# Performance work log

Measured on AMD Instinct MI355X. Metric: run time of the kernel, lower is better.

The kernel has to match this reference:

```python
import jax, jax.numpy as jnp
from jax import lax
import numpy as np

C_LL = 16      # c = 4**(px_num-1), px_num=2
C_FT = 64      # 4**px_num channels in wavelet feature ft0/ft1
TILE = C_FT // 4


def _conv3(x, w, b):
    # 3x3, stride 1, pad 1 conv in NCHW/OIHW layout
    y = lax.conv_general_dilated(x, w, (1, 1), ((1, 1), (1, 1)),
                                 dimension_numbers=('NCHW', 'OIHW', 'NCHW'))
    return y + b[None, :, None, None]


def setup_inputs() -> dict:
    key = jax.random.key(0)
    ks = jax.random.split(key, 16)
    B, H, W = 4, 256, 256

    def g(k, shape, scale=1.0):
        return jax.random.normal(k, shape, dtype=jnp.float32) * scale

    return {
        'ft0': g(ks[0], (B, C_FT, H, W)),
        'ft1': g(ks[1], (B, C_FT, H, W)),
        'gamma_up': g(ks[2], (B, 4, H, W)),
        'denoise_down': g(ks[3], (B, C_LL, H, W)),
        'coeff_a': jax.random.uniform(ks[4], (1, 1, 1, 1), dtype=jnp.float32),
        'coeff_b': jax.random.uniform(ks[5], (1, 1, 1, 1), dtype=jnp.float32),
        # FusionM: cin=24 -> 64 -> 64 -> 4
        'fw1': g(ks[6], (64, 24, 3, 3), 0.05), 'fb1': jnp.zeros((64,), jnp.float32),
        'fw2': g(ks[7], (64, 64, 3, 3), 0.05), 'fb2': jnp.zeros((64,), jnp.float32),
        'fw3': g(ks[8], (4, 64, 3, 3), 0.05), 'fb3': jnp.zeros((4,), jnp.float32),
        # DenoiseM: cin=100 -> 64 -> 64 -> 64
        'dw1': g(ks[9], (64, 100, 3, 3), 0.05), 'db1': jnp.zeros((64,), jnp.float32),
        'dw2': g(ks[10], (64, 64, 3, 3), 0.05), 'db2': jnp.zeros((64,), jnp.float32),
        'dw3': g(ks[11], (64, 64, 3, 3), 0.05), 'db3': jnp.zeros((64,), jnp.float32),
    }


def reference(ft0, ft1, gamma_up, denoise_down, coeff_a, coeff_b,
              fw1, fb1, fw2, fb2, fw3, fb3,
              dw1, db1, dw2, db2, dw3, db3):
    c = C_LL
    ll0 = ft0[:, :c]
    ll1 = ft1[:, :c]
    sigma_ll0 = jnp.clip(ll0[:, :c // 4], 0.0, 1.0) * coeff_a + coeff_b
    sigma_ll1 = jnp.clip(ll1[:, :c // 4], 0.0, 1.0) * coeff_a + coeff_b

    fusion_in = jnp.concatenate([jnp.abs(ll1 - ll0), gamma_up, sigma_ll1], axis=1)
    h = jax.nn.relu(_conv3(fusion_in, fw1, fb1))
    h = jax.nn.relu(_conv3(h, fw2, fb2))
    gamma = jax.nn.sigmoid(_conv3(h, fw3, fb3))          # [B,4,H,W]

    gammaM = jnp.repeat(gamma, TILE, axis=1)             # [B,64,H,W]
    fusion_out = ft0 * (1.0 - gammaM) + ft1 * gammaM
    sigma = (1.0 - gamma) ** 2 * sigma_ll0 + gamma ** 2 * sigma_ll1

    # DenoiseM
    denoise_in = jnp.concatenate([fusion_out, ll1, denoise_down, sigma], axis=1)  # [B,100,H,W]
    d = jax.nn.relu(_conv3(denoise_in, dw1, db1))
    d = jax.nn.relu(_conv3(d, dw2, db2))
    denoise_out = _conv3(d, dw3, db3)

    return fusion_out, denoise_out, gamma, sigma
```

## Files before the change

### kernel.cpp

```cpp
#include <hip/hip_runtime.h>
#include <stdint.h>

#define HW 65536

typedef __attribute__((ext_vector_type(8))) short short8;
typedef __attribute__((ext_vector_type(4))) float f32x4;
typedef unsigned short u16;

struct __align__(8) us4 { u16 x, y, z, w; };
struct __align__(16) us8 { us4 lo, hi; };

__device__ __forceinline__ u16 f2bf(float f) {
  union { float f; uint32_t u; } v; v.f = f;
  uint32_t r = v.u + 0x7FFFu + ((v.u >> 16) & 1u);
  return (u16)(r >> 16);
}

__device__ __forceinline__ us4 pack4(float a, float b, float c, float d) {
  us4 o; o.x = f2bf(a); o.y = f2bf(b); o.z = f2bf(c); o.w = f2bf(d); return o;
}

__device__ __forceinline__ void reorder_one(int idx, const float* __restrict__ src,
                                            u16* __restrict__ dst, int CO, int CI,
                                            int COp, int Cp) {
  int cc = idx & 7;
  int t = idx >> 3;
  int co = t % COp;
  int u = t / COp;
  int cgn = Cp >> 3;
  int cg = u % cgn;
  int tap = u / cgn;
  int ci = cg * 8 + cc;
  float v = 0.f;
  if (co < CO && ci < CI) v = src[(co * CI + ci) * 9 + tap];
  dst[idx] = f2bf(v);
}

__global__ void prep_k(const float* __restrict__ s1, const float* __restrict__ s2,
                       const float* __restrict__ s3, const float* __restrict__ s4,
                       const float* __restrict__ s5, const float* __restrict__ s6,
                       u16* __restrict__ d1, u16* __restrict__ d2, u16* __restrict__ d3,
                       u16* __restrict__ d4, u16* __restrict__ d5, u16* __restrict__ d6,
                       u16* __restrict__ zrow) {
  int idx = blockIdx.x * 256 + threadIdx.x;
  if (idx < 18432) { reorder_one(idx, s1, d1, 64, 24, 64, 32); return; }
  idx -= 18432;
  if (idx < 36864) { reorder_one(idx, s2, d2, 64, 64, 64, 64); return; }
  idx -= 36864;
  if (idx < 9216)  { reorder_one(idx, s3, d3, 4, 64, 16, 64); return; }
  idx -= 9216;
  if (idx < 73728) { reorder_one(idx, s4, d4, 64, 100, 64, 128); return; }
  idx -= 73728;
  if (idx < 36864) { reorder_one(idx, s5, d5, 64, 64, 64, 64); return; }
  idx -= 36864;
  if (idx < 36864) { reorder_one(idx, s6, d6, 64, 64, 64, 64); return; }
  idx -= 36864;
  zrow[idx] = 0;
}

__global__ void fusion_in_k(const float* __restrict__ ft0, const float* __restrict__ ft1,
                            const float* __restrict__ gup, const float* __restrict__ ca,
                            const float* __restrict__ cb, u16* __restrict__ fin) {
  const int p = blockIdx.x * 256 + threadIdx.x;
  const int n = p >> 16;
  const int pp = p & 65535;
  const float* b0 = ft0 + (size_t)n * 64 * HW + pp;
  const float* b1 = ft1 + (size_t)n * 64 * HW + pp;
  const float a = ca[0], bb = cb[0];
  u16* base = fin + ((size_t)(n * 256 + (pp >> 8)) * 4 * 256 + (pp & 255)) * 8;
  us8 o;
#pragma unroll
  for (int cg = 0; cg < 2; ++cg) {
    float v[8];
#pragma unroll
    for (int r = 0; r < 8; ++r) {
      const int ch = cg * 8 + r;
      v[r] = fabsf(b1[ch * HW] - b0[ch * HW]);
    }
    o.lo = pack4(v[0], v[1], v[2], v[3]);
    o.hi = pack4(v[4], v[5], v[6], v[7]);
    *(us8*)(base + cg * 2048) = o;
  }
  const float* gu = gup + (size_t)n * 4 * HW + pp;
  o.lo = pack4(gu[0], gu[HW], gu[2 * HW], gu[3 * HW]);
  o.hi = pack4(fminf(fmaxf(b1[0 * HW], 0.f), 1.f) * a + bb,
               fminf(fmaxf(b1[1 * HW], 0.f), 1.f) * a + bb,
               fminf(fmaxf(b1[2 * HW], 0.f), 1.f) * a + bb,
               fminf(fmaxf(b1[3 * HW], 0.f), 1.f) * a + bb);
  *(us8*)(base + 2 * 2048) = o;
  const us4 zz = {0, 0, 0, 0};
  o.lo = zz; o.hi = zz;
  *(us8*)(base + 3 * 2048) = o;
}

template <int CIN, int MT, int OMODE>
__global__ __launch_bounds__(512, 1) void conv3_k(
    const u16* __restrict__ in, const u16* __restrict__ wr,
    const float* __restrict__ bias, const u16* __restrict__ zrow,
    u16* __restrict__ obf, float* __restrict__ of32,
    const float* __restrict__ ft0, const float* __restrict__ ft1,
    const float* __restrict__ dd, const float* __restrict__ ca,
    const float* __restrict__ cb, float* __restrict__ fo_out,
    float* __restrict__ si_out, u16* __restrict__ din) {
  constexpr int M = MT * 16;
  constexpr int NCH = CIN / 32;
  constexpr int NREG = 16;
  constexpr int RSTR = 259;
  __shared__ __align__(16) u16 Blds[2 * NREG * RSTR * 8];
  const int tid = threadIdx.x;
  const int w = tid >> 6;
  const int lane = tid & 63;
  const int l15 = lane & 15;
  const int quad = lane >> 4;
  const int yo = w >> 2;
  const int wq = w & 3;

  const int b = blockIdx.x;
  const int i = b >> 3;
  const int n = i >> 4;
  const int ytile = ((b & 7) << 4) + (i & 15);
  const int y0 = ytile * 2;

  f32x4 acc[MT][4];
#pragma unroll
  for (int mt = 0; mt < MT; ++mt)
#pragma unroll
    for (int nt = 0; nt < 4; ++nt) acc[mt][nt] = (f32x4){0.f, 0.f, 0.f, 0.f};

  const u16* inb = in + (size_t)n * HW * CIN;
  const u16* rp[4];
#pragma unroll
  for (int r = 0; r < 4; ++r) {
    const int y2 = y0 + r - 1;
    rp[r] = (y2 >= 0 && y2 < 256) ? (inb + (size_t)y2 * 256 * CIN) : zrow;
  }
  if (tid < 64) {
    const int bf = tid >> 5;
    const int reg = (tid >> 1) & 15;
    const int sl = (tid & 1) * 257;
    *(float4*)&Blds[((bf * NREG + reg) * RSTR + sl) * 8] = (float4){0.f, 0.f, 0.f, 0.f};
  }

  auto stage = [&](int c, int bf) {
#pragma unroll
    for (int it = 0; it < 8; ++it) {
      const int reg = it * 2 + (tid >> 8);
      const int r = reg >> 2;
      const int g = reg & 3;
      const int slot = tid & 255;
      const u16* gp = rp[r] + ((size_t)(c * 4 + g) * 256 + slot) * 8;
      u16* lp = &Blds[((bf * NREG + reg) * RSTR + 1 + slot) * 8];
      __builtin_amdgcn_global_load_lds(
          (const __attribute__((address_space(1))) void*)gp,
          (__attribute__((address_space(3))) void*)lp, 16, 0, 0);
    }
  };

  stage(0, 0);

  for (int c = 0; c < NCH; ++c) {
    __syncthreads();
    const int cg0 = c * 4;
    const int bf = c & 1;
    short8 aw[6][MT];
#pragma unroll
    for (int t = 0; t < 5; ++t)
#pragma unroll
      for (int mt = 0; mt < MT; ++mt)
        aw[t][mt] = *(const short8*)(wr +
            (size_t)((t * (CIN / 8) + cg0 + quad) * M + mt * 16 + l15) * 8);
    if (c + 1 < NCH) stage(c + 1, bf ^ 1);
#pragma unroll
    for (int tap = 0; tap < 9; ++tap) {
      const int ky = tap / 3;
      const int kx = tap - ky * 3;
      if (tap < 4) {
        const int t2 = tap + 5;
        const int sl = t2 % 6;
#pragma unroll
        for (int mt = 0; mt < MT; ++mt)
          aw[sl][mt] = *(const short8*)(wr +
              (size_t)((t2 * (CIN / 8) + cg0 + quad) * M + mt * 16 + l15) * 8);
      }
      const int slcur = tap % 6;
      short8 bfrag[4];
#pragma unroll
      for (int nt = 0; nt < 4; ++nt)
        bfrag[nt] = *(const short8*)&Blds[((bf * NREG + (yo + ky) * 4 + quad) * RSTR +
                                           wq * 64 + nt * 16 + l15 + kx) * 8];
#pragma unroll
      for (int mt = 0; mt < MT; ++mt)
#pragma unroll
        for (int nt = 0; nt < 4; ++nt)
          acc[mt][nt] = __builtin_amdgcn_mfma_f32_16x16x32_bf16(aw[slcur][mt], bfrag[nt],
                                                                acc[mt][nt], 0, 0, 0);
    }
  }

  const int y = y0 + yo;
  if (OMODE == 0) {
    u16* ob = obf + ((size_t)n * 256 + y) * 256 * 64;
#pragma unroll
    for (int mt = 0; mt < MT; ++mt) {
      const int co = mt * 16 + quad * 4;
      const float b0 = bias[co], b1 = bias[co + 1], b2 = bias[co + 2], b3 = bias[co + 3];
#pragma unroll
      for (int nt = 0; nt < 4; ++nt) {
        const int pix = (wq * 4 + nt) * 16 + l15;
        f32x4 cc = acc[mt][nt];
        us4 o = pack4(fmaxf(cc[0] + b0, 0.f), fmaxf(cc[1] + b1, 0.f),
                      fmaxf(cc[2] + b2, 0.f), fmaxf(cc[3] + b3, 0.f));
        *(us4*)(ob + (size_t)((co >> 3) * 256 + pix) * 8 + (co & 7)) = o;
      }
    }
  } else if (OMODE == 1) {
#pragma unroll
    for (int mt = 0; mt < MT; ++mt) {
#pragma unroll
      for (int nt = 0; nt < 4; ++nt) {
        const int pix = (wq * 4 + nt) * 16 + l15;
        f32x4 cc = acc[mt][nt];
#pragma unroll
        for (int r = 0; r < 4; ++r) {
          const int co = mt * 16 + quad * 4 + r;
          of32[((size_t)n * 64 + co) * HW + y * 256 + pix] = cc[r] + bias[co];
        }
      }
    }
  } else {
    __syncthreads();
    float* glds = (float*)Blds;
    if (quad == 0) {
#pragma unroll
      for (int nt = 0; nt < 4; ++nt) {
        const int pix = (wq * 4 + nt) * 16 + l15;
        f32x4 cc = acc[0][nt];
        float gv[4];
#pragma unroll
        for (int r = 0; r < 4; ++r) {
          gv[r] = 1.f / (1.f + expf(-(cc[r] + bias[r])));
          of32[((size_t)n * 4 + r) * HW + y * 256 + pix] = gv[r];
        }
        *(f32x4*)&glds[((size_t)yo * 256 + pix) * 4] =
            (f32x4){gv[0], gv[1], gv[2], gv[3]};
      }
    }
    __syncthreads();
    const int yo2 = tid >> 8;
    const int xx = tid & 255;
    const int yy = y0 + yo2;
    const int pp = yy * 256 + xx;
    const float* b0 = ft0 + (size_t)n * 64 * HW + pp;
    const float* b1 = ft1 + (size_t)n * 64 * HW + pp;
    float* fo = fo_out + (size_t)n * 64 * HW + pp;
    const float a = ca[0], bb = cb[0];
    float g[4];
    {
      f32x4 gv = *(const f32x4*)&glds[((size_t)yo2 * 256 + xx) * 4];
      g[0] = gv[0]; g[1] = gv[1]; g[2] = gv[2]; g[3] = gv[3];
    }
    u16* dbase = din + ((size_t)(n * 256 + yy) * 16 * 256 + xx) * 8;
    us8 o;
#pragma unroll
    for (int cg = 0; cg < 8; ++cg) {
      const float gg = g[cg >> 1];
      float v[8];
#pragma unroll
      for (int r = 0; r < 8; ++r) {
        const int ch = cg * 8 + r;
        const float f0 = b0[ch * HW];
        const float f1 = b1[ch * HW];
        const float x = f0 + gg * (f1 - f0);
        fo[ch * HW] = x;
        v[r] = x;
      }
      o.lo = pack4(v[0], v[1], v[2], v[3]);
      o.hi = pack4(v[4], v[5], v[6], v[7]);
      *(us8*)(dbase + cg * 2048) = o;
    }
#pragma unroll
    for (int cg = 0; cg < 2; ++cg) {
      o.lo = pack4(b1[(cg * 8 + 0) * HW], b1[(cg * 8 + 1) * HW],
                   b1[(cg * 8 + 2) * HW], b1[(cg * 8 + 3) * HW]);
      o.hi = pack4(b1[(cg * 8 + 4) * HW], b1[(cg * 8 + 5) * HW],
                   b1[(cg * 8 + 6) * HW], b1[(cg * 8 + 7) * HW]);
      *(us8*)(dbase + (8 + cg) * 2048) = o;
    }
    const float* dn = dd + (size_t)n * 16 * HW + pp;
#pragma unroll
    for (int cg = 0; cg < 2; ++cg) {
      o.lo = pack4(dn[(cg * 8 + 0) * HW], dn[(cg * 8 + 1) * HW],
                   dn[(cg * 8 + 2) * HW], dn[(cg * 8 + 3) * HW]);
      o.hi = pack4(dn[(cg * 8 + 4) * HW], dn[(cg * 8 + 5) * HW],
                   dn[(cg * 8 + 6) * HW], dn[(cg * 8 + 7) * HW]);
      *(us8*)(dbase + (10 + cg) * 2048) = o;
    }
    float s[4];
#pragma unroll
    for (int j = 0; j < 4; ++j) {
      const float f0 = b0[j * HW], f1 = b1[j * HW];
      const float sl0 = fminf(fmaxf(f0, 0.f), 1.f) * a + bb;
      const float sl1 = fminf(fmaxf(f1, 0.f), 1.f) * a + bb;
      const float om = 1.f - g[j];
      s[j] = om * om * sl0 + g[j] * g[j] * sl1;
      si_out[((size_t)n * 4 + j) * HW + pp] = s[j];
    }
    const us4 zz = {0, 0, 0, 0};
    o.lo = pack4(s[0], s[1], s[2], s[3]);
    o.hi = zz;
    *(us8*)(dbase + 12 * 2048) = o;
    o.lo = zz;
#pragma unroll
    for (int cg = 13; cg < 16; ++cg) *(us8*)(dbase + cg * 2048) = o;
  }
}

extern "C" void kernel_launch(void* const* d_in, const int* in_sizes, int n_in,
                              void* d_out, int out_size, void* d_ws, size_t ws_size,
                              hipStream_t stream) {
  (void)in_sizes; (void)n_in; (void)out_size; (void)ws_size;
  const float* ft0 = (const float*)d_in[0];
  const float* ft1 = (const float*)d_in[1];
  const float* gup = (const float*)d_in[2];
  const float* dd  = (const float*)d_in[3];
  const float* ca  = (const float*)d_in[4];
  const float* cb  = (const float*)d_in[5];
  const float* fw1 = (const float*)d_in[6];  const float* fb1 = (const float*)d_in[7];
  const float* fw2 = (const float*)d_in[8];  const float* fb2 = (const float*)d_in[9];
  const float* fw3 = (const float*)d_in[10]; const float* fb3 = (const float*)d_in[11];
  const float* dw1 = (const float*)d_in[12]; const float* db1 = (const float*)d_in[13];
  const float* dw2 = (const float*)d_in[14]; const float* db2 = (const float*)d_in[15];
  const float* dw3 = (const float*)d_in[16]; const float* db3 = (const float*)d_in[17];

  float* out = (float*)d_out;
  float* fo_out = out;
  float* do_out = out + (size_t)4 * 64 * HW;
  float* ga_out = out + (size_t)8 * 64 * HW;
  float* si_out = ga_out + (size_t)4 * 4 * HW;

  char* ws = (char*)d_ws;
  u16* WR1 = (u16*)(ws);
  u16* WR2 = (u16*)(ws + 36864);
  u16* WR3 = (u16*)(ws + 110592);
  u16* WD1 = (u16*)(ws + 129024);
  u16* WD2 = (u16*)(ws + 276480);
  u16* WD3 = (u16*)(ws + 350208);
  u16* ZROW = (u16*)(ws + 425984);
  u16* FIN = (u16*)(ws + (1 << 20));
  u16* H1  = (u16*)(ws + 17825792);
  u16* H2  = (u16*)(ws + 51380224);
  u16* DIN = (u16*)do_out;

  dim3 blk(256);
  prep_k<<<956, blk, 0, stream>>>(fw1, fw2, fw3, dw1, dw2, dw3,
                                  WR1, WR2, WR3, WD1, WD2, WD3, ZROW);

  dim3 cblk(512);
  fusion_in_k<<<1024, blk, 0, stream>>>(ft0, ft1, gup, ca, cb, FIN);
  conv3_k<32, 4, 0><<<512, cblk, 0, stream>>>(FIN, WR1, fb1, ZROW, H1, nullptr,
      nullptr, nullptr, nullptr, nullptr, nullptr, nullptr, nullptr, nullptr);
  conv3_k<64, 4, 0><<<512, cblk, 0, stream>>>(H1, WR2, fb2, ZROW, H2, nullptr,
      nullptr, nullptr, nullptr, nullptr, nullptr, nullptr, nullptr, nullptr);
  conv3_k<64, 1, 2><<<512, cblk, 0, stream>>>(H2, WR3, fb3, ZROW, nullptr, ga_out,
      ft0, ft1, dd, ca, cb, fo_out, si_out, DIN);
  conv3_k<128, 4, 0><<<512, cblk, 0, stream>>>(DIN, WD1, db1, ZROW, H1, nullptr,
      nullptr, nullptr, nullptr, nullptr, nullptr, nullptr, nullptr, nullptr);
  conv3_k<64, 4, 0><<<512, cblk, 0, stream>>>(H1, WD2, db2, ZROW, H2, nullptr,
      nullptr, nullptr, nullptr, nullptr, nullptr, nullptr, nullptr, nullptr);
  conv3_k<64, 4, 1><<<512, cblk, 0, stream>>>(H2, WD3, db3, ZROW, nullptr, do_out,
      nullptr, nullptr, nullptr, nullptr, nullptr, nullptr, nullptr, nullptr);
}
```

Measured before the change: 487.6 us.

## Single-buffer conv LDS tile, raise occupancy bound, fold fusion input into prep

```diff
diff --git a/kernel.cpp b/kernel.cpp
--- a/kernel.cpp
+++ b/kernel.cpp
@@ -36,12 +36,52 @@
   dst[idx] = f2bf(v);
 }
 
+__device__ __forceinline__ void fusion_in_one(int p, const float* __restrict__ ft0,
+                                              const float* __restrict__ ft1,
+                                              const float* __restrict__ gup,
+                                              const float* __restrict__ ca,
+                                              const float* __restrict__ cb,
+                                              u16* __restrict__ fin) {
+  const int n = p >> 16;
+  const int pp = p & 65535;
+  const float* b0 = ft0 + (size_t)n * 64 * HW + pp;
+  const float* b1 = ft1 + (size_t)n * 64 * HW + pp;
+  const float a = ca[0], bb = cb[0];
+  u16* base = fin + ((size_t)(n * 256 + (pp >> 8)) * 4 * 256 + (pp & 255)) * 8;
+  us8 o;
+#pragma unroll
+  for (int cg = 0; cg < 2; ++cg) {
+    float v[8];
+#pragma unroll
+    for (int r = 0; r < 8; ++r) {
+      const int ch = cg * 8 + r;
+      v[r] = fabsf(b1[ch * HW] - b0[ch * HW]);
+    }
+    o.lo = pack4(v[0], v[1], v[2], v[3]);
+    o.hi = pack4(v[4], v[5], v[6], v[7]);
+    *(us8*)(base + cg * 2048) = o;
+  }
+  const float* gu = gup + (size_t)n * 4 * HW + pp;
+  o.lo = pack4(gu[0], gu[HW], gu[2 * HW], gu[3 * HW]);
+  o.hi = pack4(fminf(fmaxf(b1[0 * HW], 0.f), 1.f) * a + bb,
+               fminf(fmaxf(b1[1 * HW], 0.f), 1.f) * a + bb,
+               fminf(fmaxf(b1[2 * HW], 0.f), 1.f) * a + bb,
+               fminf(fmaxf(b1[3 * HW], 0.f), 1.f) * a + bb);
+  *(us8*)(base + 2 * 2048) = o;
+  const us4 zz = {0, 0, 0, 0};
+  o.lo = zz; o.hi = zz;
+  *(us8*)(base + 3 * 2048) = o;
+}
+
 __global__ void prep_k(const float* __restrict__ s1, const float* __restrict__ s2,
                        const float* __restrict__ s3, const float* __restrict__ s4,
                        const float* __restrict__ s5, const float* __restrict__ s6,
                        u16* __restrict__ d1, u16* __restrict__ d2, u16* __restrict__ d3,
                        u16* __restrict__ d4, u16* __restrict__ d5, u16* __restrict__ d6,
-                       u16* __restrict__ zrow) {
+                       u16* __restrict__ zrow,
+                       const float* __restrict__ ft0, const float* __restrict__ ft1,
+                       const float* __restrict__ gup, const float* __restrict__ ca,
+                       const float* __restrict__ cb, u16* __restrict__ fin) {
   int idx = blockIdx.x * 256 + threadIdx.x;
   if (idx < 18432) { reorder_one(idx, s1, d1, 64, 24, 64, 32); return; }
   idx -= 18432;
@@ -55,46 +95,13 @@
   idx -= 36864;
   if (idx < 36864) { reorder_one(idx, s6, d6, 64, 64, 64, 64); return; }
   idx -= 36864;
-  zrow[idx] = 0;
-}
-
-__global__ void fusion_in_k(const float* __restrict__ ft0, const float* __restrict__ ft1,
-                            const float* __restrict__ gup, const float* __restrict__ ca,
-                            const float* __restrict__ cb, u16* __restrict__ fin) {
-  const int p = blockIdx.x * 256 + threadIdx.x;
-  const int n = p >> 16;
-  const int pp = p & 65535;
-  const float* b0 = ft0 + (size_t)n * 64 * HW + pp;
-  const float* b1 = ft1 + (size_t)n * 64 * HW + pp;
-  const float a = ca[0], bb = cb[0];
-  u16* base = fin + ((size_t)(n * 256 + (pp >> 8)) * 4 * 256 + (pp & 255)) * 8;
-  us8 o;
-#pragma unroll
-  for (int cg = 0; cg < 2; ++cg) {
-    float v[8];
-#pragma unroll
-    for (int r = 0; r < 8; ++r) {
-      const int ch = cg * 8 + r;
-      v[r] = fabsf(b1[ch * HW] - b0[ch * HW]);
-    }
-    o.lo = pack4(v[0], v[1], v[2], v[3]);
-    o.hi = pack4(v[4], v[5], v[6], v[7]);
-    *(us8*)(base + cg * 2048) = o;
-  }
-  const float* gu = gup + (size_t)n * 4 * HW + pp;
-  o.lo = pack4(gu[0], gu[HW], gu[2 * HW], gu[3 * HW]);
-  o.hi = pack4(fminf(fmaxf(b1[0 * HW], 0.f), 1.f) * a + bb,
-               fminf(fmaxf(b1[1 * HW], 0.f), 1.f) * a + bb,
-               fminf(fmaxf(b1[2 * HW], 0.f), 1.f) * a + bb,
-               fminf(fmaxf(b1[3 * HW], 0.f), 1.f) * a + bb);
-  *(us8*)(base + 2 * 2048) = o;
-  const us4 zz = {0, 0, 0, 0};
-  o.lo = zz; o.hi = zz;
-  *(us8*)(base + 3 * 2048) = o;
+  if (idx < 32768) { zrow[idx] = 0; return; }
+  idx -= 32768;
+  fusion_in_one(idx, ft0, ft1, gup, ca, cb, fin);
 }
 
 template <int CIN, int MT, int OMODE>
-__global__ __launch_bounds__(512, 1) void conv3_k(
+__global__ __launch_bounds__(512, 4) void conv3_k(
     const u16* __restrict__ in, const u16* __restrict__ wr,
     const float* __restrict__ bias, const u16* __restrict__ zrow,
     u16* __restrict__ obf, float* __restrict__ of32,
@@ -106,7 +113,7 @@
   constexpr int NCH = CIN / 32;
   constexpr int NREG = 16;
   constexpr int RSTR = 259;
-  __shared__ __align__(16) u16 Blds[2 * NREG * RSTR * 8];
+  __shared__ __align__(16) u16 Blds[NREG * RSTR * 8];
   const int tid = threadIdx.x;
   const int w = tid >> 6;
   const int lane = tid & 63;
@@ -134,14 +141,13 @@
     const int y2 = y0 + r - 1;
     rp[r] = (y2 >= 0 && y2 < 256) ? (inb + (size_t)y2 * 256 * CIN) : zrow;
   }
-  if (tid < 64) {
-    const int bf = tid >> 5;
-    const int reg = (tid >> 1) & 15;
+  if (tid < 32) {
+    const int reg = tid >> 1;
     const int sl = (tid & 1) * 257;
-    *(float4*)&Blds[((bf * NREG + reg) * RSTR + sl) * 8] = (float4){0.f, 0.f, 0.f, 0.f};
-  }
-
-  auto stage = [&](int c, int bf) {
+    *(float4*)&Blds[((size_t)reg * RSTR + sl) * 8] = (float4){0.f, 0.f, 0.f, 0.f};
+  }
+
+  auto stage = [&](int c) {
 #pragma unroll
     for (int it = 0; it < 8; ++it) {
       const int reg = it * 2 + (tid >> 8);
@@ -149,19 +155,17 @@
       const int g = reg & 3;
       const int slot = tid & 255;
       const u16* gp = rp[r] + ((size_t)(c * 4 + g) * 256 + slot) * 8;
-      u16* lp = &Blds[((bf * NREG + reg) * RSTR + 1 + slot) * 8];
+      u16* lp = &Blds[((size_t)reg * RSTR + 1 + slot) * 8];
       __builtin_amdgcn_global_load_lds(
           (const __attribute__((address_space(1))) void*)gp,
           (__attribute__((address_space(3))) void*)lp, 16, 0, 0);
     }
   };
 
-  stage(0, 0);
+  stage(0);
 
   for (int c = 0; c < NCH; ++c) {
-    __syncthreads();
     const int cg0 = c * 4;
-    const int bf = c & 1;
     short8 aw[6][MT];
 #pragma unroll
     for (int t = 0; t < 5; ++t)
@@ -169,7 +173,7 @@
       for (int mt = 0; mt < MT; ++mt)
         aw[t][mt] = *(const short8*)(wr +
             (size_t)((t * (CIN / 8) + cg0 + quad) * M + mt * 16 + l15) * 8);
-    if (c + 1 < NCH) stage(c + 1, bf ^ 1);
+    __syncthreads();
 #pragma unroll
     for (int tap = 0; tap < 9; ++tap) {
       const int ky = tap / 3;
@@ -186,7 +190,7 @@
       short8 bfrag[4];
 #pragma unroll
       for (int nt = 0; nt < 4; ++nt)
-        bfrag[nt] = *(const short8*)&Blds[((bf * NREG + (yo + ky) * 4 + quad) * RSTR +
+        bfrag[nt] = *(const short8*)&Blds[(((size_t)(yo + ky) * 4 + quad) * RSTR +
                                            wq * 64 + nt * 16 + l15 + kx) * 8];
 #pragma unroll
       for (int mt = 0; mt < MT; ++mt)
@@ -194,6 +198,10 @@
         for (int nt = 0; nt < 4; ++nt)
           acc[mt][nt] = __builtin_amdgcn_mfma_f32_16x16x32_bf16(aw[slcur][mt], bfrag[nt],
                                                                 acc[mt][nt], 0, 0, 0);
+    }
+    if (c + 1 < NCH) {
+      __syncthreads();
+      stage(c + 1);
     }
   }
 
@@ -352,11 +360,11 @@
   u16* DIN = (u16*)do_out;
 
   dim3 blk(256);
-  prep_k<<<956, blk, 0, stream>>>(fw1, fw2, fw3, dw1, dw2, dw3,
-                                  WR1, WR2, WR3, WD1, WD2, WD3, ZROW);
+  prep_k<<<1980, blk, 0, stream>>>(fw1, fw2, fw3, dw1, dw2, dw3,
+                                   WR1, WR2, WR3, WD1, WD2, WD3, ZROW,
+                                   ft0, ft1, gup, ca, cb, FIN);
 
   dim3 cblk(512);
-  fusion_in_k<<<1024, blk, 0, stream>>>(ft0, ft1, gup, ca, cb, FIN);
   conv3_k<32, 4, 0><<<512, cblk, 0, stream>>>(FIN, WR1, fb1, ZROW, H1, nullptr,
       nullptr, nullptr, nullptr, nullptr, nullptr, nullptr, nullptr, nullptr);
   conv3_k<64, 4, 0><<<512, cblk, 0, stream>>>(H1, WR2, fb2, ZROW, H2, nullptr,
```

After: 777.9 us. 1.6x slower.
